# Kernel optimization log

Measured on AMD Instinct MI355X. Metric: run time of the kernel, lower is better.

## Reference

```python
import jax, jax.numpy as jnp
import numpy as np

DIM = 1024          # dim_feature
NUM_CLUSTERS = 8
N_PER = 4096        # patches per cluster (equal-size clusters)
NUM_SAMPLE = 1024   # num_sample_feature
QDIM = 128          # q projection dim
# sample_ratio = NUM_SAMPLE / (NUM_CLUSTERS*N_PER) = 1/32 -> top_k per cluster
TOPK = int(np.rint(N_PER * NUM_SAMPLE / (NUM_CLUSTERS * N_PER)))  # 128


def setup_inputs() -> dict:
    key = jax.random.key(0)
    ks = jax.random.split(key, 6)
    s = 1.0 / np.sqrt(DIM)
    return {
        "cluster_features": jax.random.normal(ks[0], (NUM_CLUSTERS, N_PER, DIM), jnp.float32),
        "key_feats": jax.random.normal(ks[1], (NUM_CLUSTERS, 1, DIM), jnp.float32),
        "q_w": jax.random.normal(ks[2], (QDIM, DIM), jnp.float32) * s,
        "q_b": jax.random.normal(ks[3], (QDIM,), jnp.float32) * 0.01,
        "v_w": jax.random.normal(ks[4], (DIM, DIM), jnp.float32) * s,
        "v_b": jax.random.normal(ks[5], (DIM,), jnp.float32) * 0.01,
    }


def reference(cluster_features, key_feats, q_w, q_b, v_w, v_b):
    scale_q = jnp.sqrt(jnp.float32(QDIM))

    def per_cluster(feats, key_feat):
        # NonLocalRanking with top_k=TOPK, top_fuse=False (adaptive path)
        Q = feats @ q_w.T + q_b            # [N, 128]
        qk = key_feat @ q_w.T + q_b        # [1, 128]
        A = (Q @ qk.T) / scale_q           # [N, 1]
        A = jax.nn.softmax(A, axis=0)      # softmax over patches (dim 0)
        _, idx = jax.lax.top_k(A[:, 0], TOPK)
        top_feats = feats[idx]             # [TOPK, DIM]
        V = feats @ v_w.T + v_b            # [N, DIM]
        fusion = (A.T @ V)[0]              # [DIM]
        return top_feats, fusion

    tops, fus = jax.vmap(per_cluster)(cluster_features, key_feats)
    selected = tops.reshape(-1, DIM)       # [NUM_CLUSTERS*TOPK, DIM] == [NUM_SAMPLE, DIM]
    # module pads/truncates to NUM_SAMPLE; here it is exactly NUM_SAMPLE
    selected = selected[:NUM_SAMPLE]
    return selected, fus
```

## Files before the change

kernel.cpp:

```cpp
#include <hip/hip_runtime.h>
#include <math.h>


#define DIM   1024
#define NC    8
#define NPER  4096
#define QD    128
#define TOPK  128
#define K1B   64

typedef unsigned long long u64;
typedef __attribute__((ext_vector_type(2))) unsigned long long ull2;

__global__ __launch_bounds__(256) void k0a_qk(
    const float* __restrict__ key_feats, const float* __restrict__ q_w,
    const float* __restrict__ q_b, float* __restrict__ qk_all)
{
    const int c = blockIdx.x, tid = threadIdx.x;
    __shared__ float part[256];
    const int k = tid >> 1, half = tid & 1;
    const float4* qr4 = (const float4*)(q_w + (size_t)k * DIM + half * 512);
    const float4* kf4 = (const float4*)(key_feats + (size_t)c * DIM + half * 512);
    float s = 0.f;
    #pragma unroll 8
    for (int j = 0; j < 128; ++j) {
        float4 a = qr4[j], b = kf4[j];
        s += a.x*b.x + a.y*b.y + a.z*b.z + a.w*b.w;
    }
    part[tid] = s;
    __syncthreads();
    if (tid < QD) qk_all[c * QD + tid] = part[2*tid] + part[2*tid+1] + q_b[tid];
}

__global__ __launch_bounds__(256) void k0b_w(
    const float* __restrict__ q_w, const float* __restrict__ qk_all,
    float* __restrict__ w_all)
{
    const int c = blockIdx.x >> 2, jc = blockIdx.x & 3;
    const int tid = threadIdx.x;
    const int j = jc * 256 + tid;
    __shared__ float qs[QD];
    if (tid < QD) qs[tid] = qk_all[c * QD + tid];
    __syncthreads();
    float s = 0.f;
    #pragma unroll 8
    for (int k = 0; k < QD; ++k)
        s += q_w[(size_t)k * DIM + j] * qs[k];
    w_all[c * DIM + j] = s * 0.08838834764831845f;
}

__global__ __launch_bounds__(256, 2) void k1_main(
    const float* __restrict__ feats, const float* __restrict__ w_all,
    u64* __restrict__ keys,
    float* __restrict__ pacc,
    float* __restrict__ pm, float* __restrict__ pz)
{
    const int c    = blockIdx.y;
    const int blk  = blockIdx.x;
    const int tid  = threadIdx.x;
    const int lane = tid & 63;
    const int wave = tid >> 6;

    const float4* w4 = (const float4*)(w_all + c * DIM);
    float4 wv[4];
    #pragma unroll
    for (int q = 0; q < 4; ++q) wv[q] = w4[lane + 64*q];

    float4 acc[4];
    #pragma unroll
    for (int q = 0; q < 4; ++q) acc[q] = make_float4(0.f, 0.f, 0.f, 0.f);
    float m = -INFINITY, Z = 0.f;

    const int wslot = blk * 4 + wave;
    const float* fc = feats + (size_t)c * NPER * DIM;

    float4 fA[4], fB[4];
    {
        const float4* f4 = (const float4*)(fc + (size_t)wslot * DIM);
        #pragma unroll
        for (int q = 0; q < 4; ++q) fA[q] = f4[lane + 64*q];
    }

    #define K1_PROCESS(FREG, ROW)                                              \
    do {                                                                       \
        float p = 0.f;                                                         \
        _Pragma("unroll")                                                      \
        for (int q = 0; q < 4; ++q)                                            \
            p += FREG[q].x*wv[q].x + FREG[q].y*wv[q].y +                       \
                 FREG[q].z*wv[q].z + FREG[q].w*wv[q].w;                        \
        _Pragma("unroll")                                                      \
        for (int off = 32; off > 0; off >>= 1) p += __shfl_xor(p, off, 64);    \
        if (lane == 0) {                                                       \
            unsigned int b = __float_as_uint(p);                               \
            unsigned int u = b ^ ((b & 0x80000000u) ? 0xFFFFFFFFu : 0x80000000u); \
            keys[c * NPER + (ROW)] = ((u64)u << 32) | (unsigned int)(~(ROW));  \
        }                                                                      \
        const float mn   = fmaxf(m, p);                                        \
        const float sOld = __expf(m - mn);                                     \
        const float t    = __expf(p - mn);                                     \
        Z = Z * sOld + t;                                                      \
        _Pragma("unroll")                                                      \
        for (int q = 0; q < 4; ++q) {                                          \
            acc[q].x = acc[q].x * sOld + t * FREG[q].x;                        \
            acc[q].y = acc[q].y * sOld + t * FREG[q].y;                        \
            acc[q].z = acc[q].z * sOld + t * FREG[q].z;                        \
            acc[q].w = acc[q].w * sOld + t * FREG[q].w;                        \
        }                                                                      \
        m = mn;                                                                \
    } while (0)

    for (int it = 0; it < 16; it += 2) {
        const int r0 = wslot + 256 * it;
        {
            const float4* f4 = (const float4*)(fc + (size_t)(r0 + 256) * DIM);
            #pragma unroll
            for (int q = 0; q < 4; ++q) fB[q] = f4[lane + 64*q];
        }
        K1_PROCESS(fA, r0);
        if (it + 2 < 16) {
            const float4* f4 = (const float4*)(fc + (size_t)(r0 + 512) * DIM);
            #pragma unroll
            for (int q = 0; q < 4; ++q) fA[q] = f4[lane + 64*q];
        }
        K1_PROCESS(fB, r0 + 256);
    }
    #undef K1_PROCESS

    __shared__ float sm[4], sz[4];
    __shared__ float sacc[4][DIM];
    if (lane == 0) { sm[wave] = m; sz[wave] = Z; }
    #pragma unroll
    for (int q = 0; q < 4; ++q)
        ((float4*)sacc[wave])[lane + 64*q] = acc[q];
    __syncthreads();

    const float mb = fmaxf(fmaxf(sm[0], sm[1]), fmaxf(sm[2], sm[3]));
    const float e0 = __expf(sm[0] - mb), e1 = __expf(sm[1] - mb);
    const float e2 = __expf(sm[2] - mb), e3 = __expf(sm[3] - mb);
    float4 a0 = ((float4*)sacc[0])[tid];
    float4 a1 = ((float4*)sacc[1])[tid];
    float4 a2 = ((float4*)sacc[2])[tid];
    float4 a3 = ((float4*)sacc[3])[tid];
    float4 o;
    o.x = a0.x*e0 + a1.x*e1 + a2.x*e2 + a3.x*e3;
    o.y = a0.y*e0 + a1.y*e1 + a2.y*e2 + a3.y*e3;
    o.z = a0.z*e0 + a1.z*e1 + a2.z*e2 + a3.z*e3;
    o.w = a0.w*e0 + a1.w*e1 + a2.w*e2 + a3.w*e3;
    ((float4*)(pacc + (size_t)(c * K1B + blk) * DIM))[tid] = o;
    if (tid == 0) {
        pm[c * K1B + blk] = mb;
        pz[c * K1B + blk] = sz[0]*e0 + sz[1]*e1 + sz[2]*e2 + sz[3]*e3;
    }
}

__global__ __launch_bounds__(256) void k2_combine(
    const float* __restrict__ pacc, const float* __restrict__ pm,
    const float* __restrict__ pz, float* __restrict__ g)
{
    const int c = blockIdx.x, tid = threadIdx.x;
    float mc = -INFINITY;
    for (int b = 0; b < K1B; ++b) mc = fmaxf(mc, pm[c*K1B + b]);
    float zc = 0.f;
    for (int b = 0; b < K1B; ++b) zc += pz[c*K1B + b] * __expf(pm[c*K1B + b] - mc);
    float4 s = make_float4(0.f, 0.f, 0.f, 0.f);
    for (int b = 0; b < K1B; ++b) {
        const float e = __expf(pm[c*K1B + b] - mc);
        float4 a = ((const float4*)(pacc + (size_t)(c*K1B + b) * DIM))[tid];
        s.x += e*a.x; s.y += e*a.y; s.z += e*a.z; s.w += e*a.w;
    }
    const float inv = 1.0f / zc;
    s.x *= inv; s.y *= inv; s.z *= inv; s.w *= inv;
    ((float4*)(g + c * DIM))[tid] = s;
}

__global__ __launch_bounds__(256) void k3a_rank(
    const u64* __restrict__ keys, int* __restrict__ part)
{
    const int iblk = blockIdx.x, js = blockIdx.y, c = blockIdx.z;
    const int tid = threadIdx.x;
    __shared__ u64 lk[512];
    ((float4*)lk)[tid] = ((const float4*)(keys + c * NPER + js * 512))[tid];

    const int ibase = iblk * 1024;
    u64 ki[4];
    #pragma unroll
    for (int q = 0; q < 4; ++q) ki[q] = keys[c * NPER + ibase + tid + 256*q];
    __syncthreads();

    int cnt0 = 0, cnt1 = 0, cnt2 = 0, cnt3 = 0;
    const ull2* lk2 = (const ull2*)lk;
    #pragma unroll 4
    for (int jt = 0; jt < 256; ++jt) {
        ull2 kj = lk2[jt];
        cnt0 += (kj.x > ki[0]) + (kj.y > ki[0]);
        cnt1 += (kj.x > ki[1]) + (kj.y > ki[1]);
        cnt2 += (kj.x > ki[2]) + (kj.y > ki[2]);
        cnt3 += (kj.x > ki[3]) + (kj.y > ki[3]);
    }
    int* dst = part + ((js * NC + c) << 12) + ibase + tid;
    dst[0]   = cnt0; dst[256] = cnt1; dst[512] = cnt2; dst[768] = cnt3;
}

__global__ __launch_bounds__(256) void k3b_scatter(
    const int* __restrict__ part, int* __restrict__ sel)
{
    const int c = blockIdx.y;
    const int i = blockIdx.x * 256 + threadIdx.x;
    int r = 0;
    #pragma unroll
    for (int js = 0; js < 8; ++js) r += part[((js * NC + c) << 12) + i];
    if (r < TOPK) sel[c * TOPK + r] = i;
}

__global__ __launch_bounds__(256) void k4_gather(
    const float* __restrict__ feats, const int* __restrict__ sel,
    float* __restrict__ out_sel)
{
    const int b = blockIdx.x;
    const int c = b >> 7;
    const int i = sel[b];
    const float4* src = (const float4*)(feats + ((size_t)c * NPER + i) * DIM);
    float4* dst = (float4*)(out_sel + (size_t)b * DIM);
    dst[threadIdx.x] = src[threadIdx.x];
}

__global__ __launch_bounds__(256) void k5_fusion(
    const float* __restrict__ v_w, const float* __restrict__ v_b,
    const float* __restrict__ g, float* __restrict__ fus)
{
    const int c    = blockIdx.y;
    const int tid  = threadIdx.x;
    const int lane = tid & 63;
    const int wave = tid >> 6;

    const float4* g4 = (const float4*)(g + c * DIM);
    float4 gv[4];
    #pragma unroll
    for (int q = 0; q < 4; ++q) gv[q] = g4[lane + 64*q];

    const int obase = blockIdx.x * 16 + wave * 4;
    for (int q = 0; q < 4; ++q) {
        const int o = obase + q;
        const float4* vr = (const float4*)(v_w + (size_t)o * DIM);
        float p = 0.f;
        #pragma unroll
        for (int u = 0; u < 4; ++u) {
            float4 a = vr[lane + 64*u];
            p += a.x*gv[u].x + a.y*gv[u].y + a.z*gv[u].z + a.w*gv[u].w;
        }
        #pragma unroll
        for (int off = 32; off > 0; off >>= 1)
            p += __shfl_xor(p, off, 64);
        if (lane == 0) fus[c * DIM + o] = p + v_b[o];
    }
}

extern "C" void kernel_launch(void* const* d_in, const int* in_sizes, int n_in,
                              void* d_out, int out_size, void* d_ws, size_t ws_size,
                              hipStream_t stream) {
    const float* feats     = (const float*)d_in[0];
    const float* key_feats = (const float*)d_in[1];
    const float* q_w       = (const float*)d_in[2];
    const float* q_b       = (const float*)d_in[3];
    const float* v_w       = (const float*)d_in[4];
    const float* v_b       = (const float*)d_in[5];
    float* out      = (float*)d_out;
    float* out_sel  = out;
    float* out_fus  = out + (size_t)1024 * 1024;

    u64*   keys   = (u64*)d_ws;
    float* pacc   = (float*)(keys + NC * NPER);
    float* pm     = pacc + (size_t)NC * K1B * DIM;
    float* pz     = pm + NC * K1B;
    float* g      = pz + NC * K1B;
    float* qk_all = g + NC * DIM;
    float* w_all  = qk_all + NC * QD;
    int*   part   = (int*)(w_all + NC * DIM);
    int*   sel    = part + 8 * NC * NPER;

    k0a_qk     <<<dim3(NC),           256, 0, stream>>>(key_feats, q_w, q_b, qk_all);
    k0b_w      <<<dim3(NC * 4),       256, 0, stream>>>(q_w, qk_all, w_all);
    k1_main    <<<dim3(K1B, NC),      256, 0, stream>>>(feats, w_all, keys, pacc, pm, pz);
    k2_combine <<<dim3(NC),           256, 0, stream>>>(pacc, pm, pz, g);
    k3a_rank   <<<dim3(4, 8, NC),     256, 0, stream>>>(keys, part);
    k3b_scatter<<<dim3(16, NC),       256, 0, stream>>>(part, sel);
    k4_gather  <<<dim3(NC * TOPK),    256, 0, stream>>>(feats, sel, out_sel);
    k5_fusion  <<<dim3(64, NC),       256, 0, stream>>>(v_w, v_b, g, out_fus);
}
```

Before: 271.5 us.

## Fuse prep kernels, double k1 grid, parallelize combine, batch fusion across clusters

Merges the two small query-projection kernels into one, recomputing qk redundantly in each of the four column blocks so one launch is saved. Doubles the k1 block count, halving rows per block and raising the occupancy hint, for more parallelism in the main streaming pass over feats. Spreads the combine step over more blocks and splits the partial reduction across waves. Rewrites the v_w matvec so each row of v_w is read once and applied to all eight clusters, instead of being re-read per cluster. The cost is twice as many partial accumulators to write and reduce, plus redundant qk work in the prep kernel.

```diff
diff --git a/kernel.cpp b/kernel.cpp
--- a/kernel.cpp
+++ b/kernel.cpp
@@ -7,49 +7,45 @@
 #define NPER  4096
 #define QD    128
 #define TOPK  128
-#define K1B   64
+#define K1B   128
 
 typedef unsigned long long u64;
 typedef __attribute__((ext_vector_type(2))) unsigned long long ull2;
 
-__global__ __launch_bounds__(256) void k0a_qk(
+__global__ __launch_bounds__(256) void k0_prep(
     const float* __restrict__ key_feats, const float* __restrict__ q_w,
-    const float* __restrict__ q_b, float* __restrict__ qk_all)
-{
-    const int c = blockIdx.x, tid = threadIdx.x;
+    const float* __restrict__ q_b, float* __restrict__ w_all)
+{
+    const int c  = blockIdx.x >> 2, jc = blockIdx.x & 3;
+    const int tid = threadIdx.x;
     __shared__ float part[256];
-    const int k = tid >> 1, half = tid & 1;
-    const float4* qr4 = (const float4*)(q_w + (size_t)k * DIM + half * 512);
-    const float4* kf4 = (const float4*)(key_feats + (size_t)c * DIM + half * 512);
+    __shared__ float qs[QD];
+
+    {
+        const int k = tid >> 1, half = tid & 1;
+        const float4* qr4 = (const float4*)(q_w + (size_t)k * DIM + half * 512);
+        const float4* kf4 = (const float4*)(key_feats + (size_t)c * DIM + half * 512);
+        float s = 0.f;
+        #pragma unroll 16
+        for (int j = 0; j < 128; ++j) {
+            float4 a = qr4[j], b = kf4[j];
+            s += a.x*b.x + a.y*b.y + a.z*b.z + a.w*b.w;
+        }
+        part[tid] = s;
+    }
+    __syncthreads();
+    if (tid < QD) qs[tid] = part[2*tid] + part[2*tid+1] + q_b[tid];
+    __syncthreads();
+
+    const int j = jc * 256 + tid;
     float s = 0.f;
-    #pragma unroll 8
-    for (int j = 0; j < 128; ++j) {
-        float4 a = qr4[j], b = kf4[j];
-        s += a.x*b.x + a.y*b.y + a.z*b.z + a.w*b.w;
-    }
-    part[tid] = s;
-    __syncthreads();
-    if (tid < QD) qk_all[c * QD + tid] = part[2*tid] + part[2*tid+1] + q_b[tid];
-}
-
-__global__ __launch_bounds__(256) void k0b_w(
-    const float* __restrict__ q_w, const float* __restrict__ qk_all,
-    float* __restrict__ w_all)
-{
-    const int c = blockIdx.x >> 2, jc = blockIdx.x & 3;
-    const int tid = threadIdx.x;
-    const int j = jc * 256 + tid;
-    __shared__ float qs[QD];
-    if (tid < QD) qs[tid] = qk_all[c * QD + tid];
-    __syncthreads();
-    float s = 0.f;
-    #pragma unroll 8
+    #pragma unroll 16
     for (int k = 0; k < QD; ++k)
         s += q_w[(size_t)k * DIM + j] * qs[k];
     w_all[c * DIM + j] = s * 0.08838834764831845f;
 }
 
-__global__ __launch_bounds__(256, 2) void k1_main(
+__global__ __launch_bounds__(256, 4) void k1_main(
     const float* __restrict__ feats, const float* __restrict__ w_all,
     u64* __restrict__ keys,
     float* __restrict__ pacc,
@@ -109,20 +105,20 @@
         m = mn;                                                                \
     } while (0)
 
-    for (int it = 0; it < 16; it += 2) {
-        const int r0 = wslot + 256 * it;
+    for (int it = 0; it < 8; it += 2) {
+        const int r0 = wslot + 512 * it;
         {
-            const float4* f4 = (const float4*)(fc + (size_t)(r0 + 256) * DIM);
+            const float4* f4 = (const float4*)(fc + (size_t)(r0 + 512) * DIM);
             #pragma unroll
             for (int q = 0; q < 4; ++q) fB[q] = f4[lane + 64*q];
         }
         K1_PROCESS(fA, r0);
-        if (it + 2 < 16) {
-            const float4* f4 = (const float4*)(fc + (size_t)(r0 + 512) * DIM);
+        if (it + 2 < 8) {
+            const float4* f4 = (const float4*)(fc + (size_t)(r0 + 1024) * DIM);
             #pragma unroll
             for (int q = 0; q < 4; ++q) fA[q] = f4[lane + 64*q];
         }
-        K1_PROCESS(fB, r0 + 256);
+        K1_PROCESS(fB, r0 + 512);
     }
     #undef K1_PROCESS
 
@@ -157,20 +153,48 @@
     const float* __restrict__ pacc, const float* __restrict__ pm,
     const float* __restrict__ pz, float* __restrict__ g)
 {
-    const int c = blockIdx.x, tid = threadIdx.x;
+    const int c = blockIdx.y, jb = blockIdx.x;
+    const int tid  = threadIdx.x;
+    const int slot = tid & 63;
+    const int bg   = tid >> 6;
+    __shared__ float spm[K1B], spz[K1B], swe[K1B];
+    __shared__ float szc;
+    __shared__ float4 sred[3][64];
+
+    if (tid < K1B) spm[tid] = pm[c*K1B + tid];
+    else spz[tid - K1B] = pz[c*K1B + tid - K1B];
+    __syncthreads();
     float mc = -INFINITY;
-    for (int b = 0; b < K1B; ++b) mc = fmaxf(mc, pm[c*K1B + b]);
-    float zc = 0.f;
-    for (int b = 0; b < K1B; ++b) zc += pz[c*K1B + b] * __expf(pm[c*K1B + b] - mc);
-    float4 s = make_float4(0.f, 0.f, 0.f, 0.f);
-    for (int b = 0; b < K1B; ++b) {
-        const float e = __expf(pm[c*K1B + b] - mc);
-        float4 a = ((const float4*)(pacc + (size_t)(c*K1B + b) * DIM))[tid];
-        s.x += e*a.x; s.y += e*a.y; s.z += e*a.z; s.w += e*a.w;
-    }
-    const float inv = 1.0f / zc;
-    s.x *= inv; s.y *= inv; s.z *= inv; s.w *= inv;
-    ((float4*)(g + c * DIM))[tid] = s;
+    for (int b = 0; b < K1B; ++b) mc = fmaxf(mc, spm[b]);
+    if (tid < K1B) swe[tid] = __expf(spm[tid] - mc);
+    __syncthreads();
+    if (tid == 0) {
+        float z = 0.f;
+        for (int b = 0; b < K1B; ++b) z += spz[b] * swe[b];
+        szc = z;
+    }
+
+    const int jbase = jb * 256 + slot * 4;
+    float4 a = make_float4(0.f, 0.f, 0.f, 0.f);
+    #pragma unroll
+    for (int k = 0; k < 32; ++k) {
+        const int b = bg * 32 + k;
+        const float e = swe[b];
+        float4 v = *(const float4*)(pacc + (size_t)(c*K1B + b) * DIM + jbase);
+        a.x += e*v.x; a.y += e*v.y; a.z += e*v.z; a.w += e*v.w;
+    }
+    if (bg) sred[bg-1][slot] = a;
+    __syncthreads();
+    if (bg == 0) {
+        float4 t0 = sred[0][slot], t1 = sred[1][slot], t2 = sred[2][slot];
+        const float inv = 1.0f / szc;
+        float4 o;
+        o.x = (a.x + t0.x + t1.x + t2.x) * inv;
+        o.y = (a.y + t0.y + t1.y + t2.y) * inv;
+        o.z = (a.z + t0.z + t1.z + t2.z) * inv;
+        o.w = (a.w + t0.w + t1.w + t2.w) * inv;
+        *(float4*)(g + c * DIM + jbase) = o;
+    }
 }
 
 __global__ __launch_bounds__(256) void k3a_rank(
@@ -228,30 +252,40 @@
     const float* __restrict__ v_w, const float* __restrict__ v_b,
     const float* __restrict__ g, float* __restrict__ fus)
 {
-    const int c    = blockIdx.y;
-    const int tid  = threadIdx.x;
-    const int lane = tid & 63;
-    const int wave = tid >> 6;
-
-    const float4* g4 = (const float4*)(g + c * DIM);
-    float4 gv[4];
-    #pragma unroll
-    for (int q = 0; q < 4; ++q) gv[q] = g4[lane + 64*q];
-
-    const int obase = blockIdx.x * 16 + wave * 4;
-    for (int q = 0; q < 4; ++q) {
-        const int o = obase + q;
+    __shared__ float4 sg[NC][256];
+    const int tid = threadIdx.x, lane = tid & 63, wave = tid >> 6;
+    for (int t = tid; t < NC * 256; t += 256)
+        ((float4*)sg)[t] = ((const float4*)g)[t];
+    __syncthreads();
+
+    const int row0 = blockIdx.x * 8 + wave * 2;
+    for (int rr = 0; rr < 2; ++rr) {
+        const int o = row0 + rr;
         const float4* vr = (const float4*)(v_w + (size_t)o * DIM);
-        float p = 0.f;
+        float4 v[4];
         #pragma unroll
-        for (int u = 0; u < 4; ++u) {
-            float4 a = vr[lane + 64*u];
-            p += a.x*gv[u].x + a.y*gv[u].y + a.z*gv[u].z + a.w*gv[u].w;
-        }
+        for (int u = 0; u < 4; ++u) v[u] = vr[lane + 64*u];
+        float p[NC];
         #pragma unroll
-        for (int off = 32; off > 0; off >>= 1)
-            p += __shfl_xor(p, off, 64);
-        if (lane == 0) fus[c * DIM + o] = p + v_b[o];
+        for (int cc = 0; cc < NC; ++cc) {
+            float s = 0.f;
+            #pragma unroll
+            for (int u = 0; u < 4; ++u) {
+                float4 gv = sg[cc][lane + 64*u];
+                s += v[u].x*gv.x + v[u].y*gv.y + v[u].z*gv.z + v[u].w*gv.w;
+            }
+            p[cc] = s;
+        }
+        #pragma unroll
+        for (int off = 32; off > 0; off >>= 1) {
+            #pragma unroll
+            for (int cc = 0; cc < NC; ++cc) p[cc] += __shfl_xor(p[cc], off, 64);
+        }
+        if (lane == 0) {
+            const float b = v_b[o];
+            #pragma unroll
+            for (int cc = 0; cc < NC; ++cc) fus[cc * DIM + o] = p[cc] + b;
+        }
     }
 }
 
@@ -273,17 +307,15 @@
     float* pm     = pacc + (size_t)NC * K1B * DIM;
     float* pz     = pm + NC * K1B;
     float* g      = pz + NC * K1B;
-    float* qk_all = g + NC * DIM;
-    float* w_all  = qk_all + NC * QD;
+    float* w_all  = g + NC * DIM;
     int*   part   = (int*)(w_all + NC * DIM);
     int*   sel    = part + 8 * NC * NPER;
 
-    k0a_qk     <<<dim3(NC),           256, 0, stream>>>(key_feats, q_w, q_b, qk_all);
-    k0b_w      <<<dim3(NC * 4),       256, 0, stream>>>(q_w, qk_all, w_all);
-    k1_main    <<<dim3(K1B, NC),      256, 0, stream>>>(feats, w_all, keys, pacc, pm, pz);
-    k2_combine <<<dim3(NC),           256, 0, stream>>>(pacc, pm, pz, g);
-    k3a_rank   <<<dim3(4, 8, NC),     256, 0, stream>>>(keys, part);
-    k3b_scatter<<<dim3(16, NC),       256, 0, stream>>>(part, sel);
-    k4_gather  <<<dim3(NC * TOPK),    256, 0, stream>>>(feats, sel, out_sel);
-    k5_fusion  <<<dim3(64, NC),       256, 0, stream>>>(v_w, v_b, g, out_fus);
-}
+    k0_prep    <<<dim3(NC * 4),    256, 0, stream>>>(key_feats, q_w, q_b, w_all);
+    k1_main    <<<dim3(K1B, NC),   256, 0, stream>>>(feats, w_all, keys, pacc, pm, pz);
+    k2_combine <<<dim3(4, NC),     256, 0, stream>>>(pacc, pm, pz, g);
+    k3a_rank   <<<dim3(4, 8, NC),  256, 0, stream>>>(keys, part);
+    k3b_scatter<<<dim3(16, NC),    256, 0, stream>>>(part, sel);
+    k4_gather  <<<dim3(NC * TOPK), 256, 0, stream>>>(feats, sel, out_sel);
+    k5_fusion  <<<dim3(128),       256, 0, stream>>>(v_w, v_b, g, out_fus);
+}
```

Result: no change. 275.1 us (+1.3%).
